# Performance work log

Hardware: AMD Instinct MI355X
Metric: run time of the kernel (lower is better)

The kernel has to match this reference:

```python
import jax, jax.numpy as jnp
import numpy as np

H, HKV, DH = 16, 8, 128
G = H // HKV
EPS = 1e-6
ROPE_THETA = 1000000.0


def _rms_norm(x, w):
    # RMSNorm over last dim (head_dim)
    var = jnp.mean(x * x, axis=-1, keepdims=True)
    return x * jax.lax.rsqrt(var + EPS) * w


def _rotate_half(x):
    x1, x2 = jnp.split(x, 2, axis=-1)
    return jnp.concatenate([-x2, x1], axis=-1)


def setup_inputs() -> dict:
    key = jax.random.key(0)
    ks = jax.random.split(key, 5)
    B, T, D = 2, 2048, 2048
    s = 0.02
    return {
        "x": jax.random.normal(ks[0], (B, T, D), jnp.float32),
        "wq": jax.random.normal(ks[1], (H * DH, D), jnp.float32) * s,
        "wk": jax.random.normal(ks[2], (HKV * DH, D), jnp.float32) * s,
        "wv": jax.random.normal(ks[3], (HKV * DH, D), jnp.float32) * s,
        "wo": jax.random.normal(ks[4], (D, H * DH), jnp.float32) * s,
        "q_norm_w": jnp.ones((DH,), jnp.float32),
        "k_norm_w": jnp.ones((DH,), jnp.float32),
    }


def reference(x, wq, wk, wv, wo, q_norm_w, k_norm_w):
    B, T, D = x.shape
    # projections (nn.Linear: y = x @ W^T)
    q = (x @ wq.T).reshape(B, T, H, DH).transpose(0, 2, 1, 3)      # [B,H,T,Dh]
    k = (x @ wk.T).reshape(B, T, HKV, DH).transpose(0, 2, 1, 3)    # [B,Hkv,T,Dh]
    v = (x @ wv.T).reshape(B, T, HKV, DH).transpose(0, 2, 1, 3)    # [B,Hkv,T,Dh]

    # QK RMSNorm
    q = _rms_norm(q, q_norm_w)
    k = _rms_norm(k, k_norm_w)

    # RoPE (half-split style), positions 0..T-1
    inv_freq = 1.0 / (ROPE_THETA ** (jnp.arange(0, DH, 2, dtype=jnp.float32) / DH))
    freqs = jnp.arange(T, dtype=jnp.float32)[:, None] * inv_freq[None, :]   # [T,Dh/2]
    emb = jnp.concatenate([freqs, freqs], axis=-1)                           # [T,Dh]
    cos = jnp.cos(emb)[None, None, :, :]
    sin = jnp.sin(emb)[None, None, :, :]
    q = q * cos + _rotate_half(q) * sin
    k = k * cos + _rotate_half(k) * sin

    # GQA attention with fp32 scores and causal mask
    qg = q.reshape(B, HKV, G, T, DH)
    scores = jnp.einsum("bhgtd,bhkd->bhgtk", qg.astype(jnp.float32),
                        k.astype(jnp.float32)) / jnp.sqrt(jnp.float32(DH))
    causal = jnp.tril(jnp.ones((T, T), dtype=bool))[None, None, None, :, :]
    scores = jnp.where(causal, scores, jnp.finfo(jnp.float32).min)
    attn = jax.nn.softmax(scores, axis=-1).astype(x.dtype)
    ctx = jnp.einsum("bhgtk,bhkd->bhgtd", attn, v)                            # [B,Hkv,G,T,Dh]
    out = ctx.reshape(B, H, T, DH).transpose(0, 2, 1, 3).reshape(B, T, H * DH)
    return out @ wo.T
```

## Files before the change

### kernel.cpp

```cpp
#include <hip/hip_runtime.h>
#include <cstdint>

#define Hq 16
#define HKVn 8
#define DHn 128
#define Tn 2048
#define Bn 2
#define Dm 2048
#define BT (Bn*Tn)

typedef __attribute__((ext_vector_type(8))) short bfrag8;
typedef __attribute__((ext_vector_type(4))) float facc4;
typedef __attribute__((ext_vector_type(4))) _Float16 f16x4;
typedef __attribute__((ext_vector_type(8))) _Float16 f16x8;
typedef __attribute__((ext_vector_type(8))) unsigned short us8;

__device__ __forceinline__ unsigned short f2bf(float f) {
    union { float f; unsigned int u; } v; v.f = f;
    unsigned int u = v.u;
    unsigned int r = (u + 0x7FFFu + ((u >> 16) & 1u)) >> 16;
    return (unsigned short)r;
}
__device__ __forceinline__ float bf2f(unsigned short u) {
    union { unsigned int u; float f; } v; v.u = ((unsigned int)u) << 16;
    return v.f;
}

__global__ __launch_bounds__(256) void cvt_all(const float* __restrict__ x,
                                               const float* __restrict__ wq,
                                               const float* __restrict__ wk,
                                               const float* __restrict__ wv,
                                               const float* __restrict__ wo,
                                               unsigned short* __restrict__ x_bf,
                                               unsigned short* __restrict__ wqkv_bf,
                                               unsigned short* __restrict__ wo_bf,
                                               float* __restrict__ lut) {
    int i = blockIdx.x * 256 + threadIdx.x;
    if (i >= 5242880) {
        int ii = i - 5242880;
        int t = ii >> 6, d = ii & 63;
        float fr = exp2f(-(float)d * 0.3114307588956902f);
        float ang = (float)t * fr;
        float sv, cv;
        __sincosf(ang, &sv, &cv);
        lut[t * 128 + d] = cv;
        lut[t * 128 + 64 + d] = sv;
        return;
    }
    const float4* src; ushort4* dst;
    if (i < 2097152)      { src = (const float4*)x  + i;            dst = (ushort4*)x_bf + i; }
    else if (i < 3145728) { src = (const float4*)wq + (i-2097152);  dst = (ushort4*)wqkv_bf + (i-2097152); }
    else if (i < 3670016) { src = (const float4*)wk + (i-3145728);  dst = (ushort4*)wqkv_bf + 1048576 + (i-3145728); }
    else if (i < 4194304) { src = (const float4*)wv + (i-3670016);  dst = (ushort4*)wqkv_bf + 1572864 + (i-3670016); }
    else                  { src = (const float4*)wo + (i-4194304);  dst = (ushort4*)wo_bf + (i-4194304); }
    float4 v = *src;
    ushort4 y;
    y.x = f2bf(v.x); y.y = f2bf(v.y); y.z = f2bf(v.z); y.w = f2bf(v.w);
    *dst = y;
}

__device__ __forceinline__ size_t koff_tiled(int t, int d) {
    int kc = (t >> 4) & 3, l15 = t & 15;
    int f = d >> 5, qd = (d >> 3) & 3, j = d & 7;
    return (size_t)(t >> 6) * 8192 + ((((kc * 4 + f) * 64 + qd * 16 + l15) << 3) + j);
}

__global__ __launch_bounds__(256) void gemm_bt(const unsigned short* __restrict__ A,
                                               const unsigned short* __restrict__ Bm,
                                               float* __restrict__ C,
                                               int M, int N, int K) {
    __shared__ char smem[32768];
    int tid = threadIdx.x;
    int w = tid >> 6, lane = tid & 63, quad = lane >> 4, l15 = lane & 15;
    int wr = w >> 1, wc = w & 1;
    int rowBase = blockIdx.y * 128, colBase = blockIdx.x * 128;
    facc4 acc[4][4];
#pragma unroll
    for (int i = 0; i < 4; i++)
#pragma unroll
        for (int j = 0; j < 4; j++) acc[i][j] = facc4{0.f, 0.f, 0.f, 0.f};

    for (int k0 = 0; k0 < K; k0 += 64) {
        __syncthreads();
#pragma unroll
        for (int i4 = 0; i4 < 4; i4++) {
            int c = i4 * 256 + tid;
            int r = c >> 3, kkg = (c & 7) ^ (r & 7);
            const unsigned short* ga = A + (size_t)(rowBase + r) * K + k0 + kkg * 8;
            __builtin_amdgcn_global_load_lds((const __attribute__((address_space(1))) void*)ga,
                (__attribute__((address_space(3))) void*)(smem + i4 * 4096 + w * 1024), 16, 0, 0);
            const unsigned short* gb = Bm + (size_t)(colBase + r) * K + k0 + kkg * 8;
            __builtin_amdgcn_global_load_lds((const __attribute__((address_space(1))) void*)gb,
                (__attribute__((address_space(3))) void*)(smem + 16384 + i4 * 4096 + w * 1024), 16, 0, 0);
        }
        __syncthreads();
#pragma unroll
        for (int kh = 0; kh < 2; kh++) {
            bfrag8 af[4], bf[4];
#pragma unroll
            for (int i = 0; i < 4; i++) {
                int row = wr * 64 + i * 16 + l15;
                int ch = row * 8 + ((kh * 4 + quad) ^ (row & 7));
                af[i] = *(const bfrag8*)(smem + ch * 16);
            }
#pragma unroll
            for (int j = 0; j < 4; j++) {
                int row = wc * 64 + j * 16 + l15;
                int ch = row * 8 + ((kh * 4 + quad) ^ (row & 7));
                bf[j] = *(const bfrag8*)(smem + 16384 + ch * 16);
            }
#pragma unroll
            for (int i = 0; i < 4; i++)
#pragma unroll
                for (int j = 0; j < 4; j++)
                    acc[i][j] = __builtin_amdgcn_mfma_f32_16x16x32_bf16(af[i], bf[j], acc[i][j], 0, 0, 0);
        }
    }
#pragma unroll
    for (int i = 0; i < 4; i++)
#pragma unroll
        for (int j = 0; j < 4; j++)
#pragma unroll
            for (int r = 0; r < 4; r++) {
                int row = rowBase + wr * 64 + i * 16 + quad * 4 + r;
                int col = colBase + wc * 64 + j * 16 + l15;
                C[(size_t)row * N + col] = acc[i][j][r];
            }
}

__device__ __forceinline__ void stage_half(const unsigned short* __restrict__ g0,
                                           int rowBase, int k0, char* region, int h, int tid) {
#pragma unroll
    for (int s = 0; s < 2; s++) {
        int c = h * 1024 + s * 512 + tid;
        int r = c >> 3;
        int kk = (c & 7) ^ (r & 7);
        const unsigned short* g = g0 + (size_t)(rowBase + r) * 2048 + k0 + kk * 8;
        __builtin_amdgcn_global_load_lds((const __attribute__((address_space(1))) void*)g,
            (__attribute__((address_space(3))) void*)(region + c * 16), 16, 0, 0);
    }
}

__global__ __launch_bounds__(512, 2) void gemm_qkv_fused(const unsigned short* __restrict__ A,
                                                         const unsigned short* __restrict__ Bm,
                                                         const float* __restrict__ qw,
                                                         const float* __restrict__ kw,
                                                         const float* __restrict__ lut,
                                                         unsigned short* __restrict__ q_bf,
                                                         unsigned short* __restrict__ k_bf,
                                                         _Float16* __restrict__ vT) {
    __shared__ char smem[131072];
    const int NT = 32;
    int tid = threadIdx.x;
    int w = tid >> 6, lane = tid & 63, quad = lane >> 4, l15 = lane & 15;
    int wr = w >> 2, wc = w & 3;
    int u = ((blockIdx.x & 7) << 5) | (blockIdx.x >> 3);
    int bx = u & 15, by = u >> 4;
    int rowBase = by * 256, colBase = bx * 256;

    facc4 acc[8][4];
#pragma unroll
    for (int m = 0; m < 8; m++)
#pragma unroll
        for (int n = 0; n < 4; n++) acc[m][n] = facc4{0.f, 0.f, 0.f, 0.f};

    char* b0A = smem;           char* b0B = smem + 32768;
    char* b1A = smem + 65536;   char* b1B = smem + 98304;
    stage_half(A,  rowBase, 0,  b0A, 0, tid);
    stage_half(A,  rowBase, 0,  b0A, 1, tid);
    stage_half(Bm, colBase, 0,  b0B, 0, tid);
    stage_half(Bm, colBase, 0,  b0B, 1, tid);
    stage_half(A,  rowBase, 64, b1A, 0, tid);
    stage_half(A,  rowBase, 64, b1A, 1, tid);
    stage_half(Bm, colBase, 64, b1B, 0, tid);
    asm volatile("s_waitcnt vmcnt(6)" ::: "memory");
    __builtin_amdgcn_s_barrier();

    for (int t = 0; t < NT; t++) {
        __builtin_amdgcn_sched_barrier(0);
        char* bA = smem + (t & 1) * 65536;
        char* bB = bA + 32768;
        char* oA = smem + ((t & 1) ^ 1) * 65536;
        char* oB = oA + 32768;
        int k1 = (t + 1) * 64, k2 = (t + 2) * 64;
        bfrag8 a03[4][2], a47[4][2], b01[2][2], b23[2][2];

#pragma unroll
        for (int m = 0; m < 4; m++)
#pragma unroll
            for (int kh = 0; kh < 2; kh++) {
                int row = wr * 128 + m * 16 + l15;
                int ch = (kh * 4 + quad) ^ (row & 7);
                a03[m][kh] = *(const bfrag8*)(bA + row * 128 + ch * 16);
            }
#pragma unroll
        for (int n = 0; n < 2; n++)
#pragma unroll
            for (int kh = 0; kh < 2; kh++) {
                int row = wc * 64 + n * 16 + l15;
                int ch = (kh * 4 + quad) ^ (row & 7);
                b01[n][kh] = *(const bfrag8*)(bB + row * 128 + ch * 16);
            }
        if (t + 1 < NT) stage_half(Bm, colBase, k1, oB, 1, tid);
        __builtin_amdgcn_s_barrier();
        asm volatile("s_waitcnt lgkmcnt(0)" ::: "memory");
        __builtin_amdgcn_s_setprio(1);
#pragma unroll
        for (int m = 0; m < 4; m++)
#pragma unroll
            for (int n = 0; n < 2; n++)
#pragma unroll
                for (int kh = 0; kh < 2; kh++)
                    acc[m][n] = __builtin_amdgcn_mfma_f32_16x16x32_bf16(a03[m][kh], b01[n][kh], acc[m][n], 0, 0, 0);
        __builtin_amdgcn_s_setprio(0);
        __builtin_amdgcn_s_barrier();

#pragma unroll
        for (int m = 0; m < 4; m++)
#pragma unroll
            for (int kh = 0; kh < 2; kh++) {
                int row = wr * 128 + (4 + m) * 16 + l15;
                int ch = (kh * 4 + quad) ^ (row & 7);
                a47[m][kh] = *(const bfrag8*)(bA + row * 128 + ch * 16);
            }
        __builtin_amdgcn_s_barrier();
        asm volatile("s_waitcnt lgkmcnt(0)" ::: "memory");
        __builtin_amdgcn_s_setprio(1);
#pragma unroll
        for (int m = 0; m < 4; m++)
#pragma unroll
            for (int n = 0; n < 2; n++)
#pragma unroll
                for (int kh = 0; kh < 2; kh++)
                    acc[4 + m][n] = __builtin_amdgcn_mfma_f32_16x16x32_bf16(a47[m][kh], b01[n][kh], acc[4 + m][n], 0, 0, 0);
        __builtin_amdgcn_s_setprio(0);
        __builtin_amdgcn_s_barrier();

#pragma unroll
        for (int n = 0; n < 2; n++)
#pragma unroll
            for (int kh = 0; kh < 2; kh++) {
                int row = wc * 64 + (2 + n) * 16 + l15;
                int ch = (kh * 4 + quad) ^ (row & 7);
                b23[n][kh] = *(const bfrag8*)(bB + row * 128 + ch * 16);
            }
        if (t + 2 < NT) {
            stage_half(A, rowBase, k2, bA, 0, tid);
            stage_half(A, rowBase, k2, bA, 1, tid);
        }
        __builtin_amdgcn_s_barrier();
        asm volatile("s_waitcnt lgkmcnt(0)" ::: "memory");
        __builtin_amdgcn_s_setprio(1);
#pragma unroll
        for (int m = 0; m < 4; m++)
#pragma unroll
            for (int n = 0; n < 2; n++)
#pragma unroll
                for (int kh = 0; kh < 2; kh++)
                    acc[4 + m][2 + n] = __builtin_amdgcn_mfma_f32_16x16x32_bf16(a47[m][kh], b23[n][kh], acc[4 + m][2 + n], 0, 0, 0);
        __builtin_amdgcn_s_setprio(0);
        __builtin_amdgcn_s_barrier();

        if (t + 2 < NT) stage_half(Bm, colBase, k2, bB, 0, tid);
        if (t == NT - 2)      { asm volatile("s_waitcnt vmcnt(0)" ::: "memory"); }
        else if (t < NT - 2)  { asm volatile("s_waitcnt vmcnt(6)" ::: "memory"); }
        __builtin_amdgcn_s_barrier();
        __builtin_amdgcn_s_setprio(1);
#pragma unroll
        for (int m = 0; m < 4; m++)
#pragma unroll
            for (int n = 0; n < 2; n++)
#pragma unroll
                for (int kh = 0; kh < 2; kh++)
                    acc[m][2 + n] = __builtin_amdgcn_mfma_f32_16x16x32_bf16(a03[m][kh], b23[n][kh], acc[m][2 + n], 0, 0, 0);
        __builtin_amdgcn_s_setprio(0);
        __builtin_amdgcn_s_barrier();
    }

    if (bx >= 12) {
        int hv = (bx - 12) * 2 + (wc >> 1);
#pragma unroll
        for (int half = 0; half < 2; half++) {
            int gt0 = rowBase + wr * 128 + half * 64;
            int bb = gt0 >> 11, t64 = (gt0 & 2047) >> 6;
            _Float16* vbase = vT + ((size_t)(bb * 8 + hv) * 32 + t64) * 8192;
#pragma unroll
            for (int mm = 0; mm < 4; mm++) {
                int kcp = mm >> 1, hh = mm & 1;
#pragma unroll
                for (int n = 0; n < 4; n++) {
                    int dblk = (wc & 1) * 4 + n;
                    f16x4 pv;
#pragma unroll
                    for (int r = 0; r < 4; r++) pv[r] = (_Float16)acc[half * 4 + mm][n][r];
                    *(f16x4*)(vbase + (((dblk * 2 + kcp) * 64 + quad * 16 + l15) * 8) + hh * 4) = pv;
                }
            }
        }
        return;
    }

    const float* wn = (bx < 8) ? qw : kw;
    const float osc = (bx < 8) ? (0.08838834764831845f * 1.4426950408889634f) : 1.0f;
    float* sums = (float*)smem;
#pragma unroll
    for (int m = 0; m < 8; m++)
#pragma unroll
        for (int r = 0; r < 4; r++) {
            float s = 0.f;
#pragma unroll
            for (int n = 0; n < 4; n++) s += acc[m][n][r] * acc[m][n][r];
            s += __shfl_xor(s, 1); s += __shfl_xor(s, 2);
            s += __shfl_xor(s, 4); s += __shfl_xor(s, 8);
            if (l15 == 0) sums[wc * 256 + wr * 128 + m * 16 + quad * 4 + r] = s;
        }
    __syncthreads();
    int hw = wc >> 1;
    float inv[8][4];
#pragma unroll
    for (int m = 0; m < 8; m++)
#pragma unroll
        for (int r = 0; r < 4; r++) {
            int row = wr * 128 + m * 16 + quad * 4 + r;
            float tot = sums[(2 * hw) * 256 + row] + sums[(2 * hw + 1) * 256 + row];
            inv[m][r] = rsqrtf(tot * (1.0f / 128.0f) + 1e-6f);
        }
    __syncthreads();
    unsigned short* tileb = (unsigned short*)(smem + hw * 65536);
    float wcol[4];
#pragma unroll
    for (int n = 0; n < 4; n++) wcol[n] = wn[(wc & 1) * 64 + n * 16 + l15];
#pragma unroll
    for (int m = 0; m < 8; m++)
#pragma unroll
        for (int r = 0; r < 4; r++) {
            int row = wr * 128 + m * 16 + quad * 4 + r;
            int sw = (row & 7) << 4;
#pragma unroll
            for (int n = 0; n < 4; n++) {
                int cb = ((wc & 1) * 64 + n * 16 + l15) * 2;
                *(unsigned short*)((char*)tileb + row * 256 + (cb ^ sw)) =
                    f2bf(acc[m][n][r] * inv[m][r] * wcol[n]);
            }
        }
    __syncthreads();
    {
        int row = tid >> 1, d0 = (tid & 1) * 32;
        int gt = rowBase + row;
        int tt = gt & 2047, bb = gt >> 11;
        const float* lc = lut + tt * 128;
        int sw = (row & 7) << 4;
#pragma unroll
        for (int hh2 = 0; hh2 < 2; hh2++) {
            const char* tb = (const char*)(smem + hh2 * 65536);
            unsigned short* qrow = 0; unsigned short* kplane = 0;
            if (bx < 8) qrow = q_bf + ((size_t)(bb * 16 + bx * 2 + hh2) * 2048 + tt) * 128;
            else        kplane = k_bf + (size_t)(bb * 8 + (bx - 8) * 2 + hh2) * 2048 * 128;
#pragma unroll
            for (int dc = 0; dc < 32; dc += 8) {
                int db = d0 + dc;
                us8 n0u = *(const us8*)(tb + row * 256 + ((2 * db) ^ sw));
                us8 n1u = *(const us8*)(tb + row * 256 + ((2 * db + 128) ^ sw));
                float4 cA = *(const float4*)(lc + db), cB = *(const float4*)(lc + db + 4);
                float4 sA = *(const float4*)(lc + 64 + db), sB = *(const float4*)(lc + 64 + db + 4);
                float cv[8] = {cA.x, cA.y, cA.z, cA.w, cB.x, cB.y, cB.z, cB.w};
                float sv[8] = {sA.x, sA.y, sA.z, sA.w, sB.x, sB.y, sB.z, sB.w};
                us8 p0, p1;
#pragma unroll
                for (int e = 0; e < 8; e++) {
                    float a0 = bf2f(n0u[e]), a1 = bf2f(n1u[e]);
                    p0[e] = f2bf((a0 * cv[e] - a1 * sv[e]) * osc);
                    p1[e] = f2bf((a1 * cv[e] + a0 * sv[e]) * osc);
                }
                if (bx < 8) {
                    *(us8*)(qrow + db) = p0;
                    *(us8*)(qrow + db + 64) = p1;
                } else {
                    *(us8*)(kplane + koff_tiled(tt, db)) = p0;
                    *(us8*)(kplane + koff_tiled(tt, db + 64)) = p1;
                }
            }
        }
    }
}

__global__ __launch_bounds__(256, 2) void attn_kernel(const unsigned short* __restrict__ q_bf,
                                                      const unsigned short* __restrict__ k_glob,
                                                      const _Float16* __restrict__ v_glob,
                                                      unsigned short* __restrict__ ctx) {
    __shared__ char smem[65536];
    int tid = threadIdx.x;
    int w = tid >> 6, lane = tid & 63, quad = lane >> 4, l15 = lane & 15;
    int bid = blockIdx.x;
    int u = bid & 255, halfg = bid >> 8;
    int j = u & 7, h = (u >> 3) & 15, b = (u >> 7) & 1;
    int qblk = halfg ? j : 15 - j;
    int hkv = h >> 1;
    int qb = qblk * 128;
    int qw0 = qb + w * 32;

    const unsigned short* qp = q_bf + (size_t)(b * Hq + h) * Tn * 128;
    const unsigned short* ktile = k_glob + (size_t)(b * HKVn + hkv) * 32 * 8192;
    const _Float16* vtile = v_glob + (size_t)(b * HKVn + hkv) * 32 * 8192;

    bfrag8 qf[2][4];
#pragma unroll
    for (int g = 0; g < 2; g++) {
        int row = qw0 + g * 16 + l15;
#pragma unroll
        for (int f = 0; f < 4; f++)
            qf[g][f] = *(const bfrag8*)(qp + (size_t)row * 128 + f * 32 + quad * 8);
    }

    facc4 o0[8], o1[8];
#pragma unroll
    for (int jj = 0; jj < 8; jj++) { o0[jj] = facc4{0.f,0.f,0.f,0.f}; o1[jj] = facc4{0.f,0.f,0.f,0.f}; }
    float m0 = -__builtin_inff(), m1 = -__builtin_inff(), l0 = 0.f, l1 = 0.f;

    int nkb = qb / 64 + 2;
#pragma unroll
    for (int i = 0; i < 4; i++) {
        const unsigned short* gk = ktile + (size_t)(i * 256 + tid) * 8;
        __builtin_amdgcn_global_load_lds((const __attribute__((address_space(1))) void*)gk,
            (__attribute__((address_space(3))) void*)(smem + i * 4096 + w * 1024), 16, 0, 0);
        const _Float16* gv = vtile + (size_t)(i * 256 + tid) * 8;
        __builtin_amdgcn_global_load_lds((const __attribute__((address_space(1))) void*)gv,
            (__attribute__((address_space(3))) void*)(smem + 16384 + i * 4096 + w * 1024), 16, 0, 0);
    }

    for (int ib = 0; ib < nkb; ib++) {
        int kb = ib * 64;
        __syncthreads();
        if (ib + 1 < nkb) {
            char* nb = smem + ((ib + 1) & 1) * 32768;
#pragma unroll
            for (int i = 0; i < 4; i++) {
                const unsigned short* gk = ktile + (size_t)(ib + 1) * 8192 + (i * 256 + tid) * 8;
                __builtin_amdgcn_global_load_lds((const __attribute__((address_space(1))) void*)gk,
                    (__attribute__((address_space(3))) void*)(nb + i * 4096 + w * 1024), 16, 0, 0);
                const _Float16* gv = vtile + (size_t)(ib + 1) * 8192 + (i * 256 + tid) * 8;
                __builtin_amdgcn_global_load_lds((const __attribute__((address_space(1))) void*)gv,
                    (__attribute__((address_space(3))) void*)(nb + 16384 + i * 4096 + w * 1024), 16, 0, 0);
            }
        }
        char* cb = smem + (ib & 1) * 32768;
        if (kb <= qw0 + 31) {
            facc4 s0[4], s1[4];
#pragma unroll
            for (int kc = 0; kc < 4; kc++) {
                bfrag8 kf[4];
#pragma unroll
                for (int f = 0; f < 4; f++)
                    kf[f] = *(const bfrag8*)(cb + (((kc * 4 + f) * 64 + lane) << 4));
                facc4 a = facc4{0.f,0.f,0.f,0.f}, bq = facc4{0.f,0.f,0.f,0.f};
#pragma unroll
                for (int f = 0; f < 4; f++) {
                    a  = __builtin_amdgcn_mfma_f32_16x16x32_bf16(kf[f], qf[0][f], a, 0, 0, 0);
                    bq = __builtin_amdgcn_mfma_f32_16x16x32_bf16(kf[f], qf[1][f], bq, 0, 0, 0);
                }
                s0[kc] = a; s1[kc] = bq;
            }
            if (kb + 63 > qw0) {
                int q0 = qw0 + l15, q1 = q0 + 16;
#pragma unroll
                for (int kc = 0; kc < 4; kc++)
#pragma unroll
                    for (int r = 0; r < 4; r++) {
                        int k = kb + kc * 16 + quad * 4 + r;
                        if (k > q0) s0[kc][r] = -__builtin_inff();
                        if (k > q1) s1[kc][r] = -__builtin_inff();
                    }
            }
            float mx0 = s0[0][0], mx1 = s1[0][0];
#pragma unroll
            for (int kc = 0; kc < 4; kc++)
#pragma unroll
                for (int r = 0; r < 4; r++) {
                    mx0 = fmaxf(mx0, s0[kc][r]); mx1 = fmaxf(mx1, s1[kc][r]);
                }
            mx0 = fmaxf(mx0, __shfl_xor(mx0, 16)); mx0 = fmaxf(mx0, __shfl_xor(mx0, 32));
            mx1 = fmaxf(mx1, __shfl_xor(mx1, 16)); mx1 = fmaxf(mx1, __shfl_xor(mx1, 32));
            float mn0 = fmaxf(m0, mx0), mn1 = fmaxf(m1, mx1);
            float alpha0 = exp2f(m0 - mn0), alpha1 = exp2f(m1 - mn1);
            m0 = mn0; m1 = mn1;
            float rs0 = 0.f, rs1 = 0.f;
#pragma unroll
            for (int kc = 0; kc < 4; kc++)
#pragma unroll
                for (int r = 0; r < 4; r++) {
                    s0[kc][r] = exp2f(s0[kc][r] - m0); rs0 += s0[kc][r];
                    s1[kc][r] = exp2f(s1[kc][r] - m1); rs1 += s1[kc][r];
                }
            rs0 += __shfl_xor(rs0, 16); rs0 += __shfl_xor(rs0, 32);
            rs1 += __shfl_xor(rs1, 16); rs1 += __shfl_xor(rs1, 32);
            l0 = l0 * alpha0 + rs0; l1 = l1 * alpha1 + rs1;
#pragma unroll
            for (int jj = 0; jj < 8; jj++)
#pragma unroll
                for (int r = 0; r < 4; r++) { o0[jj][r] *= alpha0; o1[jj][r] *= alpha1; }
            f16x4 pb0[4], pb1[4];
#pragma unroll
            for (int kc = 0; kc < 4; kc++) {
                pb0[kc] = f16x4{(_Float16)s0[kc][0], (_Float16)s0[kc][1],
                                (_Float16)s0[kc][2], (_Float16)s0[kc][3]};
                pb1[kc] = f16x4{(_Float16)s1[kc][0], (_Float16)s1[kc][1],
                                (_Float16)s1[kc][2], (_Float16)s1[kc][3]};
            }
#pragma unroll
            for (int kcp = 0; kcp < 2; kcp++)
#pragma unroll
                for (int dblk = 0; dblk < 8; dblk++) {
                    f16x8 vv = *(const f16x8*)(cb + 16384 + (((dblk * 2 + kcp) * 64 + lane) << 4));
                    f16x4 a0 = f16x4{vv[0], vv[1], vv[2], vv[3]};
                    f16x4 a1 = f16x4{vv[4], vv[5], vv[6], vv[7]};
                    o0[dblk] = __builtin_amdgcn_mfma_f32_16x16x16f16(a0, pb0[kcp*2],   o0[dblk], 0, 0, 0);
                    o0[dblk] = __builtin_amdgcn_mfma_f32_16x16x16f16(a1, pb0[kcp*2+1], o0[dblk], 0, 0, 0);
                    o1[dblk] = __builtin_amdgcn_mfma_f32_16x16x16f16(a0, pb1[kcp*2],   o1[dblk], 0, 0, 0);
                    o1[dblk] = __builtin_amdgcn_mfma_f32_16x16x16f16(a1, pb1[kcp*2+1], o1[dblk], 0, 0, 0);
                }
        }
    }
    float inv0 = 1.0f / l0, inv1 = 1.0f / l1;
#pragma unroll
    for (int g = 0; g < 2; g++) {
        int q = qw0 + g * 16 + l15;
        float invl = g ? inv1 : inv0;
#pragma unroll
        for (int dblk = 0; dblk < 8; dblk++) {
            facc4 ov = g ? o1[dblk] : o0[dblk];
            ushort4 st;
            st.x = f2bf(ov[0] * invl); st.y = f2bf(ov[1] * invl);
            st.z = f2bf(ov[2] * invl); st.w = f2bf(ov[3] * invl);
            *(ushort4*)(ctx + ((size_t)(b * Tn + q)) * 2048 + h * 128 + dblk * 16 + quad * 4) = st;
        }
    }
}

extern "C" void kernel_launch(void* const* d_in, const int* in_sizes, int n_in,
                              void* d_out, int out_size, void* d_ws, size_t ws_size,
                              hipStream_t stream) {
    (void)in_sizes; (void)n_in; (void)out_size; (void)ws_size;
    const float* x  = (const float*)d_in[0];
    const float* wq = (const float*)d_in[1];
    const float* wk = (const float*)d_in[2];
    const float* wv = (const float*)d_in[3];
    const float* wo = (const float*)d_in[4];
    const float* qw = (const float*)d_in[5];
    const float* kw = (const float*)d_in[6];
    float* out = (float*)d_out;
    char* ws = (char*)d_ws;

    unsigned short* x_bf    = (unsigned short*)(ws);
    unsigned short* wqkv_bf = (unsigned short*)(ws + 16777216);
    unsigned short* wo_bf   = (unsigned short*)(ws + 33554432);
    unsigned short* q_bf    = (unsigned short*)(ws + 41943040);
    unsigned short* k_bf    = (unsigned short*)(ws + 58720256);
    _Float16*       vT_f16  = (_Float16*)(ws + 67108864);
    unsigned short* ctx_bf  = (unsigned short*)(ws + 75497472);
    float*          lut     = (float*)(ws + 92274688);

    cvt_all<<<20992, 256, 0, stream>>>(x, wq, wk, wv, wo, x_bf, wqkv_bf, wo_bf, lut);
    gemm_qkv_fused<<<256, 512, 0, stream>>>(x_bf, wqkv_bf, qw, kw, lut, q_bf, k_bf, vT_f16);
    attn_kernel<<<512, 256, 0, stream>>>(q_bf, k_bf, vT_f16, ctx_bf);
    gemm_bt<<<dim3(16, 32), 256, 0, stream>>>(ctx_bf, wo_bf, out, 4096, 2048, 2048);
}
```

Baseline: 318.8 us.

## Reorder GEMM quadrant schedule and prefetch next tile's fragments across iterations

Restructures the GEMM main loop so the A0-3 and B0-1 register fragments for the next k-tile are read from LDS at the end of the current iteration, and loads them once before the loop. The four MFMA quadrants are reordered so each LDS fragment load overlaps a preceding MFMA block, and the explicit lgkmcnt(0) waits are replaced with sched_barrier hints. The initial staging order changes so the B half needed first lands earlier. This aims to hide LDS read latency behind matrix math, but depends on the compiler inserting correct waits and adds register pressure from fragments that stay live across iterations.

```diff
diff --git a/kernel.cpp b/kernel.cpp
--- a/kernel.cpp
+++ b/kernel.cpp
@@ -170,11 +170,29 @@
     stage_half(A,  rowBase, 0,  b0A, 1, tid);
     stage_half(Bm, colBase, 0,  b0B, 0, tid);
     stage_half(Bm, colBase, 0,  b0B, 1, tid);
+    stage_half(Bm, colBase, 64, b1B, 0, tid);
     stage_half(A,  rowBase, 64, b1A, 0, tid);
     stage_half(A,  rowBase, 64, b1A, 1, tid);
-    stage_half(Bm, colBase, 64, b1B, 0, tid);
     asm volatile("s_waitcnt vmcnt(6)" ::: "memory");
     __builtin_amdgcn_s_barrier();
+
+    bfrag8 a03[4][2], a47[4][2], b01[2][2], b23[2][2];
+#pragma unroll
+    for (int m = 0; m < 4; m++)
+#pragma unroll
+        for (int kh = 0; kh < 2; kh++) {
+            int row = wr * 128 + m * 16 + l15;
+            int ch = (kh * 4 + quad) ^ (row & 7);
+            a03[m][kh] = *(const bfrag8*)(b0A + row * 128 + ch * 16);
+        }
+#pragma unroll
+    for (int n = 0; n < 2; n++)
+#pragma unroll
+        for (int kh = 0; kh < 2; kh++) {
+            int row = wc * 64 + n * 16 + l15;
+            int ch = (kh * 4 + quad) ^ (row & 7);
+            b01[n][kh] = *(const bfrag8*)(b0B + row * 128 + ch * 16);
+        }
 
     for (int t = 0; t < NT; t++) {
         __builtin_amdgcn_sched_barrier(0);
@@ -183,27 +201,18 @@
         char* oA = smem + ((t & 1) ^ 1) * 65536;
         char* oB = oA + 32768;
         int k1 = (t + 1) * 64, k2 = (t + 2) * 64;
-        bfrag8 a03[4][2], a47[4][2], b01[2][2], b23[2][2];
-
-#pragma unroll
-        for (int m = 0; m < 4; m++)
+
+#pragma unroll
+        for (int n = 0; n < 2; n++)
 #pragma unroll
             for (int kh = 0; kh < 2; kh++) {
-                int row = wr * 128 + m * 16 + l15;
+                int row = wc * 64 + (2 + n) * 16 + l15;
                 int ch = (kh * 4 + quad) ^ (row & 7);
-                a03[m][kh] = *(const bfrag8*)(bA + row * 128 + ch * 16);
-            }
-#pragma unroll
-        for (int n = 0; n < 2; n++)
-#pragma unroll
-            for (int kh = 0; kh < 2; kh++) {
-                int row = wc * 64 + n * 16 + l15;
-                int ch = (kh * 4 + quad) ^ (row & 7);
-                b01[n][kh] = *(const bfrag8*)(bB + row * 128 + ch * 16);
+                b23[n][kh] = *(const bfrag8*)(bB + row * 128 + ch * 16);
             }
         if (t + 1 < NT) stage_half(Bm, colBase, k1, oB, 1, tid);
-        __builtin_amdgcn_s_barrier();
-        asm volatile("s_waitcnt lgkmcnt(0)" ::: "memory");
+        __builtin_amdgcn_sched_barrier(0);
+        __builtin_amdgcn_s_barrier();
         __builtin_amdgcn_s_setprio(1);
 #pragma unroll
         for (int m = 0; m < 4; m++)
@@ -223,8 +232,42 @@
                 int ch = (kh * 4 + quad) ^ (row & 7);
                 a47[m][kh] = *(const bfrag8*)(bA + row * 128 + ch * 16);
             }
-        __builtin_amdgcn_s_barrier();
-        asm volatile("s_waitcnt lgkmcnt(0)" ::: "memory");
+        __builtin_amdgcn_sched_barrier(0);
+        __builtin_amdgcn_s_barrier();
+        __builtin_amdgcn_s_setprio(1);
+#pragma unroll
+        for (int m = 0; m < 4; m++)
+#pragma unroll
+            for (int n = 0; n < 2; n++)
+#pragma unroll
+                for (int kh = 0; kh < 2; kh++)
+                    acc[m][2 + n] = __builtin_amdgcn_mfma_f32_16x16x32_bf16(a03[m][kh], b23[n][kh], acc[m][2 + n], 0, 0, 0);
+        __builtin_amdgcn_s_setprio(0);
+        __builtin_amdgcn_s_barrier();
+
+        if (t + 2 < NT) stage_half(Bm, colBase, k2, bB, 0, tid);
+        __builtin_amdgcn_sched_barrier(0);
+        __builtin_amdgcn_s_barrier();
+        __builtin_amdgcn_s_setprio(1);
+#pragma unroll
+        for (int m = 0; m < 4; m++)
+#pragma unroll
+            for (int n = 0; n < 2; n++)
+#pragma unroll
+                for (int kh = 0; kh < 2; kh++)
+                    acc[4 + m][2 + n] = __builtin_amdgcn_mfma_f32_16x16x32_bf16(a47[m][kh], b23[n][kh], acc[4 + m][2 + n], 0, 0, 0);
+        __builtin_amdgcn_s_setprio(0);
+        __builtin_amdgcn_s_barrier();
+
+        if (t + 2 < NT) {
+            stage_half(A, rowBase, k2, bA, 0, tid);
+            stage_half(A, rowBase, k2, bA, 1, tid);
+            asm volatile("s_waitcnt vmcnt(6)" ::: "memory");
+        } else if (t + 1 < NT) {
+            asm volatile("s_waitcnt vmcnt(0)" ::: "memory");
+        }
+        __builtin_amdgcn_sched_barrier(0);
+        __builtin_amdgcn_s_barrier();
         __builtin_amdgcn_s_setprio(1);
 #pragma unroll
         for (int m = 0; m < 4; m++)
@@ -234,46 +277,24 @@
                 for (int kh = 0; kh < 2; kh++)
                     acc[4 + m][n] = __builtin_amdgcn_mfma_f32_16x16x32_bf16(a47[m][kh], b01[n][kh], acc[4 + m][n], 0, 0, 0);
         __builtin_amdgcn_s_setprio(0);
-        __builtin_amdgcn_s_barrier();
-
-#pragma unroll
-        for (int n = 0; n < 2; n++)
-#pragma unroll
-            for (int kh = 0; kh < 2; kh++) {
-                int row = wc * 64 + (2 + n) * 16 + l15;
-                int ch = (kh * 4 + quad) ^ (row & 7);
-                b23[n][kh] = *(const bfrag8*)(bB + row * 128 + ch * 16);
-            }
-        if (t + 2 < NT) {
-            stage_half(A, rowBase, k2, bA, 0, tid);
-            stage_half(A, rowBase, k2, bA, 1, tid);
-        }
-        __builtin_amdgcn_s_barrier();
-        asm volatile("s_waitcnt lgkmcnt(0)" ::: "memory");
-        __builtin_amdgcn_s_setprio(1);
-#pragma unroll
-        for (int m = 0; m < 4; m++)
+        if (t + 1 < NT) {
+#pragma unroll
+            for (int m = 0; m < 4; m++)
+#pragma unroll
+                for (int kh = 0; kh < 2; kh++) {
+                    int row = wr * 128 + m * 16 + l15;
+                    int ch = (kh * 4 + quad) ^ (row & 7);
+                    a03[m][kh] = *(const bfrag8*)(oA + row * 128 + ch * 16);
+                }
 #pragma unroll
             for (int n = 0; n < 2; n++)
 #pragma unroll
-                for (int kh = 0; kh < 2; kh++)
-                    acc[4 + m][2 + n] = __builtin_amdgcn_mfma_f32_16x16x32_bf16(a47[m][kh], b23[n][kh], acc[4 + m][2 + n], 0, 0, 0);
-        __builtin_amdgcn_s_setprio(0);
-        __builtin_amdgcn_s_barrier();
-
-        if (t + 2 < NT) stage_half(Bm, colBase, k2, bB, 0, tid);
-        if (t == NT - 2)      { asm volatile("s_waitcnt vmcnt(0)" ::: "memory"); }
-        else if (t < NT - 2)  { asm volatile("s_waitcnt vmcnt(6)" ::: "memory"); }
-        __builtin_amdgcn_s_barrier();
-        __builtin_amdgcn_s_setprio(1);
-#pragma unroll
-        for (int m = 0; m < 4; m++)
-#pragma unroll
-            for (int n = 0; n < 2; n++)
-#pragma unroll
-                for (int kh = 0; kh < 2; kh++)
-                    acc[m][2 + n] = __builtin_amdgcn_mfma_f32_16x16x32_bf16(a03[m][kh], b23[n][kh], acc[m][2 + n], 0, 0, 0);
-        __builtin_amdgcn_s_setprio(0);
+                for (int kh = 0; kh < 2; kh++) {
+                    int row = wc * 64 + n * 16 + l15;
+                    int ch = (kh * 4 + quad) ^ (row & 7);
+                    b01[n][kh] = *(const bfrag8*)(oB + row * 128 + ch * 16);
+                }
+        }
         __builtin_amdgcn_s_barrier();
     }
 
```

New measurement: 319.2 us. No clear change (+0.1%).
